# Performance work log

Measured on AMD Instinct MI355X. Metric: run time of the kernel, lower is better.

Reference implementation:

```python
import jax, jax.numpy as jnp
import numpy as np

TEMP = 0.08
EPS = 1e-8
GAMMA = 0.99
BETA = 0.5 * (1.0 - GAMMA)  # alpha * (1 - gamma)
COS_EPS = 1e-8  # torch F.cosine_similarity norm-product clamp


def setup_inputs() -> dict:
    key = jax.random.key(0)
    k1, k2, k3 = jax.random.split(key, 3)
    B, D, C = 8192, 256, 7
    features = jax.random.normal(k1, (B, D), dtype=jnp.float32)
    labels = jax.random.randint(k2, (B,), 0, C)
    # orthogonal prototypes via QR, as in generate_orthogonal_vectors
    q, _ = jnp.linalg.qr(jax.random.normal(k3, (D, C), dtype=jnp.float32))
    prototypes = q.T  # [C, D]
    momentums = jnp.zeros((C, D), dtype=jnp.float32)
    return {"features": features, "labels": labels,
            "prototypes": prototypes, "momentums": momentums}


def _update_prototypes(features, labels, prototypes, momentums):
    # sequential EMA over the batch (repeated labels chain), as in the torch loop
    deltas = features - prototypes[labels]  # delta uses the OLD prototypes throughout

    def step(m, ld):
        l, d = ld
        return m.at[l].set(GAMMA * m[l] + BETA * d), None

    m_final, _ = jax.lax.scan(step, momentums, (labels, deltas))
    target = prototypes + m_final  # [C, D]
    q, _ = jnp.linalg.qr(target.T)  # reduced QR: [D, C]
    return q.T  # [C, D], re-orthogonalized prototypes


def reference(features, labels, prototypes, momentums):
    C = prototypes.shape[0]
    new_protos = _update_prototypes(features, labels, prototypes, momentums)

    feats = jnp.concatenate([features, new_protos], axis=0)          # [N, D]
    labs = jnp.concatenate([labels, jnp.arange(C, dtype=labels.dtype)])
    N = feats.shape[0]

    # cosine similarity matrix: dot / clamp(|x||y|, eps)  (matches F.cosine_similarity)
    nrm = jnp.linalg.norm(feats, axis=-1)                            # [N]
    sim = (feats @ feats.T) / jnp.maximum(nrm[:, None] * nrm[None, :], COS_EPS)
    scores = (1.0 + sim) * 0.5 + EPS

    offdiag = 1.0 - jnp.eye(N, dtype=scores.dtype)
    scores = scores * offdiag / TEMP
    scores = scores - jnp.max(scores)

    same = labs[:, None] == labs[None, :]                            # [N, N] bool
    pos_mask = same.astype(scores.dtype) * offdiag
    neg_mask = (~same).astype(scores.dtype)

    pos = jnp.sum(scores * pos_mask, axis=-1) / (jnp.sum(pos_mask, axis=-1) + EPS)
    neg = jnp.log(jnp.sum(jnp.exp(scores) * neg_mask, axis=-1) + EPS)
    loss = -pos + neg                                                # [N]

    m = loss > 0
    cnt = jnp.sum(m.astype(loss.dtype))
    mean_pos = jnp.sum(jnp.where(m, loss, 0.0)) / jnp.maximum(cnt, 1.0)
    return jnp.where(cnt > 0, mean_pos, jnp.array(0.0, loss.dtype))
```

## Files before the change

### kernel.cpp

```cpp
#include <hip/hip_runtime.h>
#include <stdint.h>

#define B    8192
#define D    256
#define C    7
#define NTOT 8199
#define NPAD 8320
#define NT   65
#define NBLK 2145
#define BETAC 0.005f
#define L2GAMMA (-0.0144995696951151f)
#define KC   (6.25f + 1.25e-7f)
#define EC1  9.016844005555771f
#define EC0  9.016844185925551f

using f32x4  = __attribute__((ext_vector_type(4))) float;

__device__ __forceinline__ void async16(const void* src, void* dst) {
    __builtin_amdgcn_global_load_lds(
        (const __attribute__((address_space(1))) void*)src,
        (__attribute__((address_space(3))) void*)dst, 16, 0, 0);
}

#define WAITVM(N) asm volatile("s_waitcnt vmcnt(" #N ")" ::: "memory")
#define BARRIER() do { __builtin_amdgcn_s_barrier(); asm volatile("" ::: "memory"); } while(0)

__global__ void kzero(float* __restrict__ z) {
    int t = threadIdx.x;
    for (int i = t; i < 1804; i += 256) z[i] = 0.f;
}

__global__ void kaccnorm(const float* __restrict__ feats, const int* __restrict__ labels,
                         float* __restrict__ S, unsigned* __restrict__ G32,
                         int* __restrict__ labs_ext, int* __restrict__ hist) {
    __shared__ int cnt[256 * 8];
    __shared__ int tot[8];
    __shared__ float wrow[32];
    __shared__ float sacc[4][7][256];
    int tid = threadIdx.x, lane = tid & 63, wv = tid >> 6;
    int bid = blockIdx.x;

    int lab[32];
    #pragma unroll
    for (int q = 0; q < 8; ++q) {
        int4 v = *(const int4*)(labels + tid * 32 + q * 4);
        lab[q * 4 + 0] = v.x; lab[q * 4 + 1] = v.y;
        lab[q * 4 + 2] = v.z; lab[q * 4 + 3] = v.w;
    }
    int myc[8] = {0, 0, 0, 0, 0, 0, 0, 0};
    #pragma unroll
    for (int k = 0; k < 32; ++k) {
        #pragma unroll
        for (int cc = 0; cc < 7; ++cc) myc[cc] += (lab[k] == cc) ? 1 : 0;
    }
    #pragma unroll
    for (int cc = 0; cc < 8; ++cc) cnt[tid * 8 + cc] = myc[cc];
    __syncthreads();
    for (int c = wv; c < C; c += 4) {
        int v[4], partial = 0;
        #pragma unroll
        for (int k = 0; k < 4; ++k) { v[k] = cnt[(lane * 4 + k) * 8 + c]; partial += v[k]; }
        int inc = partial;
        #pragma unroll
        for (int d = 1; d < 64; d <<= 1) {
            int y = __shfl_up(inc, d);
            if (lane >= d) inc += y;
        }
        int run = inc - partial;
        #pragma unroll
        for (int k = 0; k < 4; ++k) { int tmp = v[k]; cnt[(lane * 4 + k) * 8 + c] = run; run += tmp; }
        if (lane == 63) { tot[c] = inc; if (bid == 0) hist[c] = inc; }
    }
    __syncthreads();
    if (tid == 0) {
        int loc[7];
        #pragma unroll
        for (int cc = 0; cc < 7; ++cc) loc[cc] = cnt[bid * 8 + cc];
        for (int k = 0; k < 32; ++k) {
            int c2 = labels[bid * 32 + k];
            int r = ++loc[c2];
            wrow[k] = exp2f((float)(tot[c2] - r) * L2GAMMA);
        }
    }
    if (tid < 32) labs_ext[bid * 32 + tid] = labels[bid * 32 + tid];
    if (bid == 0) {
        if (tid < 128) { int i2 = B + tid; labs_ext[i2] = (i2 < NTOT) ? (i2 - B) : -1; }
        for (int i = tid; i < 121 * 64; i += 256) G32[NTOT * 64 + i] = 0u;
    }
    __syncthreads();

    float acc7[7][4] = {};
    int base = bid * 32 + wv * 8;
    for (int k = 0; k < 8; ++k) {
        int row = base + k;
        const float4 v = *(const float4*)(feats + (size_t)row * 256 + lane * 4);
        float ss = v.x * v.x + v.y * v.y + v.z * v.z + v.w * v.w;
        #pragma unroll
        for (int off = 1; off < 64; off <<= 1) ss += __shfl_xor(ss, off);
        float rn = 1.f / sqrtf(ss);
        unsigned p = (unsigned)__builtin_amdgcn_cvt_pk_fp8_f32(v.x * rn, v.y * rn, 0, false);
        p = (unsigned)__builtin_amdgcn_cvt_pk_fp8_f32(v.z * rn, v.w * rn, (int)p, true);
        G32[(size_t)row * 64 + lane] = p;
        int c = labels[row];
        float wgt = wrow[wv * 8 + k];
        #pragma unroll
        for (int cc = 0; cc < 7; ++cc)
            if (c == cc) {
                acc7[cc][0] += wgt * v.x; acc7[cc][1] += wgt * v.y;
                acc7[cc][2] += wgt * v.z; acc7[cc][3] += wgt * v.w;
            }
    }
    #pragma unroll
    for (int cc = 0; cc < 7; ++cc)
        #pragma unroll
        for (int jj = 0; jj < 4; ++jj) sacc[wv][cc][lane * 4 + jj] = acc7[cc][jj];
    __syncthreads();
    #pragma unroll
    for (int cc = 0; cc < 7; ++cc) {
        float s = sacc[0][cc][tid] + sacc[1][cc][tid] + sacc[2][cc][tid] + sacc[3][cc][tid];
        if (s != 0.f) atomicAdd(&S[cc * 256 + tid], s);
    }
}

__global__ __launch_bounds__(512, 2) void kmain(const unsigned char* __restrict__ G,
                                                unsigned* __restrict__ G32w,
                                                const int* __restrict__ labs,
                                                float* __restrict__ pP,
                                                float* __restrict__ pN,
                                                const float* __restrict__ S,
                                                const int* __restrict__ hist,
                                                const float* __restrict__ protos,
                                                const float* __restrict__ moms,
                                                unsigned* __restrict__ flag) {
    __shared__ unsigned char Asm_[128 * 256];
    __shared__ unsigned char Bsm_[128 * 256];
    __shared__ float vvs[8];
    __shared__ float bcast[8];
    float* rowP = (float*)Asm_;
    float* rowN = rowP + 256;
    float* colP = rowN + 256;
    float* colN = colP + 512;

    int b0 = blockIdx.x;
    int xcd = b0 & 7, pos = b0 >> 3;
    int b = (xcd == 0) ? pos : (269 + (xcd - 1) * 268 + pos);

    int jt = (int)((sqrtf(8.f * (float)b + 1.f) - 1.f) * 0.5f);
    while ((jt * (jt + 1)) / 2 > b) --jt;
    while (((jt + 1) * (jt + 2)) / 2 <= b) ++jt;
    int it = b - (jt * (jt + 1)) / 2;

    int rowA = it * 128, rowB = jt * 128;
    int tid = threadIdx.x, lane = tid & 63, w8 = tid >> 6;
    int wr = w8 >> 1, wc = w8 & 1;
    int g4 = lane >> 4, q15 = lane & 15;
    const char* gb = (const char*)G;

    if (b == 0) {
        float* Aq = (float*)Asm_;
        float* Vq = (float*)Bsm_;
        int t = tid, w = tid >> 6, ln = tid & 63;
        if (tid < 256) {
            #pragma unroll
            for (int c = 0; c < C; ++c) {
                float p = protos[c * 256 + t];
                float m0 = moms[c * 256 + t];
                float gn = exp2f((float)hist[c] * L2GAMMA);
                float mf = gn * m0 + BETAC * S[c * 256 + t] - 0.5f * (1.f - gn) * p;
                Aq[t * 8 + c] = p + mf;
                Vq[t * 8 + c] = 0.f;
            }
        }
        __syncthreads();
        for (int j = 0; j < C; ++j) {
            if (tid < 64) {
                float s = 0.f;
                for (int i = tid; i < 256; i += 64) {
                    float a = (i >= j) ? Aq[i * 8 + j] : 0.f;
                    s += a * a;
                }
                #pragma unroll
                for (int off = 32; off; off >>= 1) s += __shfl_xor(s, off);
                if (tid == 0) {
                    float norm = sqrtf(s);
                    float alpha = Aq[j * 8 + j];
                    float beta = (alpha >= 0.f) ? -norm : norm;
                    float vv = 2.f * beta * (beta - alpha);
                    bcast[0] = alpha; bcast[1] = beta;
                    bcast[2] = (vv > 0.f) ? 1.f : 0.f;
                    vvs[j] = (vv > 0.f) ? vv : 1.f;
                }
            }
            __syncthreads();
            if (tid < 256) {
                float alpha = bcast[0], valid = bcast[2];
                float beta = bcast[1];
                float vi = 0.f;
                if (valid != 0.f) {
                    if (t == j) vi = alpha - beta;
                    else if (t > j) vi = Aq[t * 8 + j];
                }
                Vq[t * 8 + j] = vi;
            }
            __syncthreads();
            if (tid < 256) {
                float vvj = vvs[j];
                for (int k = j + 1 + w; k < C; k += 4) {
                    float cp = 0.f;
                    for (int i = ln; i < 256; i += 64) cp += Vq[i * 8 + j] * Aq[i * 8 + k];
                    #pragma unroll
                    for (int off = 32; off; off >>= 1) cp += __shfl_xor(cp, off);
                    float scale = 2.f * cp / vvj;
                    for (int i = ln; i < 256; i += 64) Aq[i * 8 + k] -= scale * Vq[i * 8 + j];
                }
            }
            __syncthreads();
        }
        if (tid < 256) {
            #pragma unroll
            for (int c = 0; c < C; ++c) Aq[t * 8 + c] = (t == c) ? 1.f : 0.f;
        }
        __syncthreads();
        for (int j = C - 1; j >= 0; --j) {
            if (tid < 256) {
                float vvj = vvs[j];
                for (int k = w; k < C; k += 4) {
                    float cp = 0.f;
                    for (int i = ln; i < 256; i += 64) cp += Vq[i * 8 + j] * Aq[i * 8 + k];
                    #pragma unroll
                    for (int off = 32; off; off >>= 1) cp += __shfl_xor(cp, off);
                    float scale = 2.f * cp / vvj;
                    for (int i = ln; i < 256; i += 64) Aq[i * 8 + k] -= scale * Vq[i * 8 + j];
                }
            }
            __syncthreads();
        }
        if (tid < 256) {
            for (int c = w; c < C; c += 4) {
                float s = 0.f;
                for (int i = ln; i < 256; i += 64) { float a = Aq[i * 8 + c]; s += a * a; }
                #pragma unroll
                for (int off = 32; off; off >>= 1) s += __shfl_xor(s, off);
                if (ln == 0) bcast[c] = 1.f / sqrtf(s);
            }
        }
        __syncthreads();
        if (tid < 256) {
            unsigned char* G8 = (unsigned char*)G32w;
            #pragma unroll
            for (int c = 0; c < C; ++c) {
                float val = Aq[t * 8 + c] * bcast[c];
                int pk = __builtin_amdgcn_cvt_pk_fp8_f32(val, 0.f, 0, false);
                G8[(size_t)(B + c) * 256 + t] = (unsigned char)(pk & 0xff);
            }
        }
        __syncthreads();
        if (tid == 0) { __threadfence(); atomicExch(flag, 1u); }
    }

    bool protoTile = (jt == NT - 1);
    if (protoTile) {
        if (tid == 0) {
            while (atomicAdd(flag, 0u) == 0u) __builtin_amdgcn_s_sleep(32);
        }
        __syncthreads();
    }

    #pragma unroll
    for (int q = 0; q < 4; ++q) {
        int o = q * 8192 + tid * 16;
        int row = o >> 8, colb = o & 255;
        int sc = colb ^ ((row & 15) << 4);
        async16(gb + (size_t)(rowA + row) * 256 + sc, (char*)Asm_ + o);
    }
    #pragma unroll
    for (int q = 0; q < 4; ++q) {
        int o = q * 8192 + tid * 16;
        int row = o >> 8, colb = o & 255;
        int sc = colb ^ ((row & 15) << 4);
        async16(gb + (size_t)(rowB + row) * 256 + sc, (char*)Bsm_ + o);
    }

    int ljv[4];
    #pragma unroll
    for (int n = 0; n < 4; ++n) ljv[n] = labs[rowB + wc * 64 + n * 16 + q15];
    int4 lrow[2];
    #pragma unroll
    for (int m = 0; m < 2; ++m)
        lrow[m] = *(const int4*)(labs + rowA + wr * 32 + m * 16 + g4 * 4);

    f32x4 acc[2][4];
    #pragma unroll
    for (int m = 0; m < 2; ++m)
        #pragma unroll
        for (int n = 0; n < 4; ++n) acc[m][n] = 0.f;

    WAITVM(0);
    BARRIER();

    if (protoTile) {
        if (tid < 448) {
            int c = tid >> 6, l = tid & 63;
            unsigned v = __hip_atomic_load(&G32w[(size_t)(B + c) * 64 + l],
                                           __ATOMIC_RELAXED, __HIP_MEMORY_SCOPE_AGENT);
            int off = c * 256 + ((((l >> 2) ^ c) << 4) | ((l & 3) << 2));
            *(unsigned*)((char*)Bsm_ + off) = v;
            if (it == NT - 1) *(unsigned*)((char*)Asm_ + off) = v;
        }
        __syncthreads();
    }

    #pragma unroll
    for (int kk = 0; kk < 8; ++kk) {
        long af[2], bfr[4];
        int cb = (kk * 32 + g4 * 8) ^ (q15 << 4);
        #pragma unroll
        for (int m = 0; m < 2; ++m) {
            int r0 = wr * 32 + m * 16 + q15;
            af[m] = *(const long*)((const char*)Asm_ + r0 * 256 + cb);
        }
        #pragma unroll
        for (int n = 0; n < 4; ++n) {
            int r0 = wc * 64 + n * 16 + q15;
            bfr[n] = *(const long*)((const char*)Bsm_ + r0 * 256 + cb);
        }
        __builtin_amdgcn_s_setprio(1);
        #pragma unroll
        for (int m = 0; m < 2; ++m)
            #pragma unroll
            for (int n = 0; n < 4; ++n)
                acc[m][n] = __builtin_amdgcn_mfma_f32_16x16x32_fp8_fp8(af[m], bfr[n], acc[m][n], 0, 0, 0);
        __builtin_amdgcn_s_setprio(0);
    }

    __syncthreads();

    float cs[4] = {0.f, 0.f, 0.f, 0.f}, cn[4] = {0.f, 0.f, 0.f, 0.f};
    bool fastpath = (it != jt) && (jt != NT - 1);

#define EPI(VALIDEXPR)                                                         \
    _Pragma("unroll")                                                          \
    for (int m = 0; m < 2; ++m) {                                              \
        _Pragma("unroll")                                                      \
        for (int r = 0; r < 4; ++r) {                                          \
            int il = wr * 32 + m * 16 + g4 * 4 + r;                            \
            int i = rowA + il; (void)i;                                        \
            int li = ((const int*)&lrow[m])[r];                                \
            float ps = 0.f, ns = 0.f;                                          \
            _Pragma("unroll")                                                  \
            for (int n = 0; n < 4; ++n) {                                      \
                int j = rowB + wc * 64 + n * 16 + q15; (void)j;                \
                float sim = acc[m][n][r];                                      \
                float s = fmaf(sim, 6.25f, KC);                                \
                float e = exp2f(fmaf(sim, EC1, EC0));                          \
                if (VALIDEXPR) {                                               \
                    if (li == ljv[n]) { ps += s; cs[n] += s; }                 \
                    else              { ns += e; cn[n] += e; }                 \
                }                                                              \
            }                                                                  \
            _Pragma("unroll")                                                  \
            for (int off = 1; off < 16; off <<= 1) {                           \
                ps += __shfl_xor(ps, off);                                     \
                ns += __shfl_xor(ns, off);                                     \
            }                                                                  \
            if (q15 == 0) { rowP[wc * 128 + il] = ps; rowN[wc * 128 + il] = ns; } \
        }                                                                      \
    }

    if (fastpath) { EPI(true); }
    else          { EPI(i < NTOT && j < NTOT && i != j); }
#undef EPI

    #pragma unroll
    for (int n = 0; n < 4; ++n) {
        float a = cs[n], bb = cn[n];
        a += __shfl_xor(a, 16); a += __shfl_xor(a, 32);
        bb += __shfl_xor(bb, 16); bb += __shfl_xor(bb, 32);
        if (g4 == 0) {
            colP[wr * 128 + wc * 64 + n * 16 + q15] = a;
            colN[wr * 128 + wc * 64 + n * 16 + q15] = bb;
        }
    }

    __syncthreads();
    if (tid < 128) {
        pP[(size_t)jt * NPAD + rowA + tid] = rowP[tid] + rowP[128 + tid];
        pN[(size_t)jt * NPAD + rowA + tid] = rowN[tid] + rowN[128 + tid];
    } else if (tid < 256 && it != jt) {
        int tt = tid - 128;
        pP[(size_t)it * NPAD + rowB + tt] = colP[tt] + colP[128 + tt] + colP[256 + tt] + colP[384 + tt];
        pN[(size_t)it * NPAD + rowB + tt] = colN[tt] + colN[128 + tt] + colN[256 + tt] + colN[384 + tt];
    }
}

__global__ void kreduce(const float* __restrict__ pP, const float* __restrict__ pN,
                        const int* __restrict__ hist, const int* __restrict__ labs,
                        float* __restrict__ lossacc, unsigned* __restrict__ ticket,
                        float* __restrict__ out) {
    int i = blockIdx.x * 256 + threadIdx.x;
    float lsum = 0.f, lcnt = 0.f;
    if (i < NTOT) {
        float sp = 0.f, sn = 0.f;
        #pragma unroll 5
        for (int c = 0; c < NT; ++c) {
            sp += pP[(size_t)c * NPAD + i];
            sn += pN[(size_t)c * NPAD + i];
        }
        float cnt = (float)hist[labs[i]];
        float pos = sp / (cnt + 1e-8f);
        float neg = logf(sn + 1e-8f);
        float loss = neg - pos;
        if (loss > 0.f) { lsum = loss; lcnt = 1.f; }
    }
    #pragma unroll
    for (int off = 1; off < 64; off <<= 1) {
        lsum += __shfl_xor(lsum, off);
        lcnt += __shfl_xor(lcnt, off);
    }
    __shared__ float s1[4], s2[4];
    int lane = threadIdx.x & 63, w = threadIdx.x >> 6;
    if (lane == 0) { s1[w] = lsum; s2[w] = lcnt; }
    __syncthreads();
    if (threadIdx.x == 0) {
        atomicAdd(&lossacc[0], s1[0] + s1[1] + s1[2] + s1[3]);
        atomicAdd(&lossacc[1], s2[0] + s2[1] + s2[2] + s2[3]);
        __threadfence();
        unsigned tk = atomicAdd(ticket, 1u);
        if (tk == 32) {
            float a = atomicAdd(&lossacc[0], 0.f);
            float c2 = atomicAdd(&lossacc[1], 0.f);
            out[0] = (c2 > 0.f) ? a / fmaxf(c2, 1.f) : 0.f;
        }
    }
}

extern "C" void kernel_launch(void* const* d_in, const int* in_sizes, int n_in,
                              void* d_out, int out_size, void* d_ws, size_t ws_size,
                              hipStream_t stream) {
    const float* feats  = (const float*)d_in[0];
    const int*   labels = (const int*)d_in[1];
    const float* protos = (const float*)d_in[2];
    const float* moms   = (const float*)d_in[3];
    float* out = (float*)d_out;

    char* ws = (char*)d_ws;
    float*    S_      = (float*)(ws + 0);
    int*      hist    = (int*)  (ws + 7168);
    float*    lossacc = (float*)(ws + 7200);
    unsigned* ticket  = (unsigned*)(ws + 7208);
    unsigned* flag    = (unsigned*)(ws + 7212);
    int*      labs    = (int*)  (ws + 7296);
    unsigned char* G  = (unsigned char*)(ws + 40704);
    float*    pP      = (float*)(ws + 2170624);
    float*    pN      = (float*)(ws + 4333824);

    kzero<<<1, 256, 0, stream>>>((float*)ws);
    kaccnorm<<<256, 256, 0, stream>>>(feats, labels, S_, (unsigned*)G, labs, hist);
    kmain<<<NBLK, 512, 0, stream>>>(G, (unsigned*)G, labs, pP, pN, S_, hist,
                                    protos, moms, flag);
    kreduce<<<33, 256, 0, stream>>>(pP, pN, hist, labs, lossacc, ticket, out);
}
```

Baseline: 87.49 us.

## Split K staging into two halves to halve LDS and raise occupancy

Shared A/B tiles shrink from 128x256 to 128x128 bytes. The K dimension is now staged and multiplied in two sequential halves, with a new XOR swizzle and a new prototype-row placement for each half. Launch bounds rise from 2 to 8 minimum blocks so more workgroups can be resident and hide load latency. Each block now waits on global loads twice with no double buffering, and the tighter launch bound may cap registers and cause spills.

```diff
diff --git a/kernel.cpp b/kernel.cpp
--- a/kernel.cpp
+++ b/kernel.cpp
@@ -122,7 +122,7 @@
     }
 }
 
-__global__ __launch_bounds__(512, 2) void kmain(const unsigned char* __restrict__ G,
+__global__ __launch_bounds__(512, 8) void kmain(const unsigned char* __restrict__ G,
                                                 unsigned* __restrict__ G32w,
                                                 const int* __restrict__ labs,
                                                 float* __restrict__ pP,
@@ -132,8 +132,8 @@
                                                 const float* __restrict__ protos,
                                                 const float* __restrict__ moms,
                                                 unsigned* __restrict__ flag) {
-    __shared__ unsigned char Asm_[128 * 256];
-    __shared__ unsigned char Bsm_[128 * 256];
+    __shared__ unsigned char Asm_[128 * 128];
+    __shared__ unsigned char Bsm_[128 * 128];
     __shared__ float vvs[8];
     __shared__ float bcast[8];
     float* rowP = (float*)Asm_;
@@ -259,26 +259,18 @@
     }
 
     bool protoTile = (jt == NT - 1);
+    unsigned pv = 0; int pl = 0, poff = 0;
     if (protoTile) {
         if (tid == 0) {
             while (atomicAdd(flag, 0u) == 0u) __builtin_amdgcn_s_sleep(32);
         }
         __syncthreads();
-    }
-
-    #pragma unroll
-    for (int q = 0; q < 4; ++q) {
-        int o = q * 8192 + tid * 16;
-        int row = o >> 8, colb = o & 255;
-        int sc = colb ^ ((row & 15) << 4);
-        async16(gb + (size_t)(rowA + row) * 256 + sc, (char*)Asm_ + o);
-    }
-    #pragma unroll
-    for (int q = 0; q < 4; ++q) {
-        int o = q * 8192 + tid * 16;
-        int row = o >> 8, colb = o & 255;
-        int sc = colb ^ ((row & 15) << 4);
-        async16(gb + (size_t)(rowB + row) * 256 + sc, (char*)Bsm_ + o);
+        if (tid < 448) {
+            int pc = tid >> 6; pl = tid & 63;
+            pv = __hip_atomic_load(&G32w[(size_t)(B + pc) * 64 + pl],
+                                   __ATOMIC_RELAXED, __HIP_MEMORY_SCOPE_AGENT);
+            poff = pc * 128 + (((pl & 31) << 2) ^ ((pc & 7) << 4));
+        }
     }
 
     int ljv[4];
@@ -289,49 +281,76 @@
     for (int m = 0; m < 2; ++m)
         lrow[m] = *(const int4*)(labs + rowA + wr * 32 + m * 16 + g4 * 4);
 
+#define STAGEH(H)                                                              \
+    do {                                                                       \
+        _Pragma("unroll")                                                      \
+        for (int q = 0; q < 2; ++q) {                                          \
+            int o = q * 8192 + tid * 16;                                       \
+            int row = o >> 7, colb = o & 127;                                  \
+            int sc = colb ^ ((row & 7) << 4);                                  \
+            async16(gb + (size_t)(rowA + row) * 256 + (H) * 128 + sc, (char*)Asm_ + o); \
+            async16(gb + (size_t)(rowB + row) * 256 + (H) * 128 + sc, (char*)Bsm_ + o); \
+        }                                                                      \
+    } while (0)
+
+#define MFMAH()                                                                \
+    do {                                                                       \
+        _Pragma("unroll")                                                      \
+        for (int kk = 0; kk < 4; ++kk) {                                       \
+            long af[2], bfr[4];                                                \
+            int cb = (kk * 32 + g4 * 8) ^ ((q15 & 7) << 4);                    \
+            _Pragma("unroll")                                                  \
+            for (int m = 0; m < 2; ++m) {                                      \
+                int r0 = wr * 32 + m * 16 + q15;                               \
+                af[m] = *(const long*)((const char*)Asm_ + r0 * 128 + cb);     \
+            }                                                                  \
+            _Pragma("unroll")                                                  \
+            for (int n = 0; n < 4; ++n) {                                      \
+                int r0 = wc * 64 + n * 16 + q15;                               \
+                bfr[n] = *(const long*)((const char*)Bsm_ + r0 * 128 + cb);    \
+            }                                                                  \
+            __builtin_amdgcn_s_setprio(1);                                     \
+            _Pragma("unroll")                                                  \
+            for (int m = 0; m < 2; ++m)                                        \
+                _Pragma("unroll")                                              \
+                for (int n = 0; n < 4; ++n)                                    \
+                    acc[m][n] = __builtin_amdgcn_mfma_f32_16x16x32_fp8_fp8(af[m], bfr[n], acc[m][n], 0, 0, 0); \
+            __builtin_amdgcn_s_setprio(0);                                     \
+        }                                                                      \
+    } while (0)
+
     f32x4 acc[2][4];
     #pragma unroll
     for (int m = 0; m < 2; ++m)
         #pragma unroll
         for (int n = 0; n < 4; ++n) acc[m][n] = 0.f;
 
+    STAGEH(0);
     WAITVM(0);
     BARRIER();
-
     if (protoTile) {
-        if (tid < 448) {
-            int c = tid >> 6, l = tid & 63;
-            unsigned v = __hip_atomic_load(&G32w[(size_t)(B + c) * 64 + l],
-                                           __ATOMIC_RELAXED, __HIP_MEMORY_SCOPE_AGENT);
-            int off = c * 256 + ((((l >> 2) ^ c) << 4) | ((l & 3) << 2));
-            *(unsigned*)((char*)Bsm_ + off) = v;
-            if (it == NT - 1) *(unsigned*)((char*)Asm_ + off) = v;
-        }
-        __syncthreads();
-    }
-
-    #pragma unroll
-    for (int kk = 0; kk < 8; ++kk) {
-        long af[2], bfr[4];
-        int cb = (kk * 32 + g4 * 8) ^ (q15 << 4);
-        #pragma unroll
-        for (int m = 0; m < 2; ++m) {
-            int r0 = wr * 32 + m * 16 + q15;
-            af[m] = *(const long*)((const char*)Asm_ + r0 * 256 + cb);
-        }
-        #pragma unroll
-        for (int n = 0; n < 4; ++n) {
-            int r0 = wc * 64 + n * 16 + q15;
-            bfr[n] = *(const long*)((const char*)Bsm_ + r0 * 256 + cb);
-        }
-        __builtin_amdgcn_s_setprio(1);
-        #pragma unroll
-        for (int m = 0; m < 2; ++m)
-            #pragma unroll
-            for (int n = 0; n < 4; ++n)
-                acc[m][n] = __builtin_amdgcn_mfma_f32_16x16x32_fp8_fp8(af[m], bfr[n], acc[m][n], 0, 0, 0);
-        __builtin_amdgcn_s_setprio(0);
-    }
+        if (tid < 448 && pl < 32) {
+            *(unsigned*)((char*)Bsm_ + poff) = pv;
+            if (it == NT - 1) *(unsigned*)((char*)Asm_ + poff) = pv;
+        }
+        __syncthreads();
+    }
+    MFMAH();
+    BARRIER();
+
+    STAGEH(1);
+    WAITVM(0);
+    BARRIER();
+    if (protoTile) {
+        if (tid < 448 && pl >= 32) {
+            *(unsigned*)((char*)Bsm_ + poff) = pv;
+            if (it == NT - 1) *(unsigned*)((char*)Asm_ + poff) = pv;
+        }
+        __syncthreads();
+    }
+    MFMAH();
+#undef STAGEH
+#undef MFMAH
 
     __syncthreads();
 
```

New measurement: 152.8 us. +74.6%, slower.
